# Optimization experiments

Measured on AMD Instinct MI355X. Metric: run time of the kernel, lower is better.

The kernel has to match this reference:

```python
import jax, jax.numpy as jnp
import numpy as np

NUM_HEADS = 16
HIDDEN = 1024
HEAD_DIM = HIDDEN // NUM_HEADS


def setup_inputs() -> dict:
    key = jax.random.key(0)
    ks = jax.random.split(key, 12)
    B, S, H = 4, 1024, HIDDEN
    s = 1.0 / np.sqrt(H)
    inp = {
        "aspect_hidden": jax.random.normal(ks[0], (B, S, H), jnp.float32),
        "opinion_hidden": jax.random.normal(ks[1], (B, S, H), jnp.float32),
        "attention_mask": jnp.ones((B, S), jnp.int32),
        # torch nn.Linear weights are [out, in]
        "Wq": jax.random.normal(ks[2], (H, H), jnp.float32) * s,
        "bq": jnp.zeros((H,), jnp.float32),
        "Wk": jax.random.normal(ks[3], (H, H), jnp.float32) * s,
        "bk": jnp.zeros((H,), jnp.float32),
        "Wv": jax.random.normal(ks[4], (H, H), jnp.float32) * s,
        "bv": jnp.zeros((H,), jnp.float32),
        "Wo": jax.random.normal(ks[5], (H, H), jnp.float32) * s,
        "bo": jnp.zeros((H,), jnp.float32),
        # nn.Bilinear(H, H, 1): weight [1, H, H], bias [1]
        "Wbil": jax.random.normal(ks[6], (1, H, H), jnp.float32) * s,
        "bbil": jnp.zeros((1,), jnp.float32),
    }
    return inp


def reference(aspect_hidden, opinion_hidden, attention_mask,
              Wq, bq, Wk, bk, Wv, bv, Wo, bo, Wbil, bbil):
    B, Sq, H = aspect_hidden.shape
    Sk = opinion_hidden.shape[1]
    nh, hd = NUM_HEADS, HEAD_DIM
    scale = hd ** (-0.5)

    q = (aspect_hidden @ Wq.T + bq).reshape(B, Sq, nh, hd).transpose(0, 2, 1, 3)
    k = (opinion_hidden @ Wk.T + bk).reshape(B, Sk, nh, hd).transpose(0, 2, 1, 3)
    v = (opinion_hidden @ Wv.T + bv).reshape(B, Sk, nh, hd).transpose(0, 2, 1, 3)

    # bilinear span bias: span[b,s] = a[b,s] @ Wbil[0] @ o[b,s] + bbil
    span = jnp.einsum('bsh,hk,bsk->bs', aspect_hidden, Wbil[0], opinion_hidden) + bbil[0]

    # scores [B, nh, Sq, Sk] with span bias broadcast over heads and keys
    scores = jnp.einsum('bhqd,bhkd->bhqk', q, k) * scale + span[:, None, :, None]
    scores = jnp.where(attention_mask[:, None, None, :] == 0, -jnp.inf, scores)

    probs = jax.nn.softmax(scores, axis=-1)
    ctx = jnp.einsum('bhqk,bhkd->bhqd', probs, v)
    ctx = ctx.transpose(0, 2, 1, 3).reshape(B, Sq, H)
    return ctx @ Wo.T + bo
```

## Files before the change

kernel.cpp:

```cpp
#include <hip/hip_runtime.h>
#include <hip/hip_bf16.h>
#include <stdint.h>

typedef __attribute__((ext_vector_type(4))) float f32x4;
typedef __attribute__((ext_vector_type(16))) float f32x16;
typedef __attribute__((ext_vector_type(8))) short bf16x8;
typedef __attribute__((ext_vector_type(4))) unsigned int u32x4;
typedef unsigned short u16;

#define GBL_AS1(p) ((const __attribute__((address_space(1))) void*)(p))
#define LDS_AS3(p) ((__attribute__((address_space(3))) void*)(p))

static __device__ __forceinline__ u16 f2bf(float f) {
  __hip_bfloat16 h = __float2bfloat16(f);
  union { __hip_bfloat16 h; u16 u; } c; c.h = h;
  return c.u;
}

__global__ __launch_bounds__(256) void fused_cast(
    const float* __restrict__ a, const float* __restrict__ o,
    const float* __restrict__ wq_, const float* __restrict__ wk_,
    const float* __restrict__ wv_, const float* __restrict__ wo_,
    const int* __restrict__ mask,
    u16* __restrict__ aB, u16* __restrict__ oB,
    u16* __restrict__ WqB, u16* __restrict__ WkB,
    u16* __restrict__ WvB, u16* __restrict__ WoB,
    int* __restrict__ flags) {
  if (blockIdx.x == 0 && threadIdx.x < 64) {
    int bb = threadIdx.x >> 4, kt = threadIdx.x & 15;
    int anyz = 0;
    for (int s = 0; s < 64; ++s) anyz |= (mask[bb * 1024 + kt * 64 + s] == 0);
    flags[threadIdx.x] = anyz;
  }
  int idx = blockIdx.x * 256 + threadIdx.x;
#pragma unroll
  for (int j = 0; j < 4; ++j) {
    int i = idx + j * 786432;
    const float* src; u16* dst; int off;
    if (i < 1048576) { src = a; dst = aB; off = i; }
    else if (i < 2097152) { src = o; dst = oB; off = i - 1048576; }
    else {
      int w = (i - 2097152) >> 18; off = (i - 2097152) & 262143;
      src = (w == 0) ? wq_ : (w == 1) ? wk_ : (w == 2) ? wv_ : wo_;
      dst = (w == 0) ? WqB : (w == 1) ? WkB : (w == 2) ? WvB : WoB;
    }
    float4 v = reinterpret_cast<const float4*>(src)[off];
    ushort4 ov;
    ov.x = f2bf(v.x); ov.y = f2bf(v.y); ov.z = f2bf(v.z); ov.w = f2bf(v.w);
    reinterpret_cast<ushort4*>(dst)[off] = ov;
  }
}

static __device__ __forceinline__ void gemm_core2(const u16* __restrict__ A,
                                                  const u16* __restrict__ B,
                                                  u16* lds_a, u16* lds_b,
                                                  f32x4 acc[4][4]) {
  const int tid = threadIdx.x, lane = tid & 63, wv = tid >> 6;
  const int wm = wv >> 1, wn = wv & 1;
  const int fr = lane & 15, fq = lane >> 4;

#define GSTAGE(kt_, buf_) do { \
    _Pragma("unroll") \
    for (int i_ = 0; i_ < 4; ++i_) { \
      int cb_ = (wv * 4 + i_) * 64; \
      int c_ = cb_ + lane; \
      int r_ = c_ >> 3; \
      int sc_ = ((c_ & 7) ^ (r_ & 7)) * 8; \
      __builtin_amdgcn_global_load_lds(GBL_AS1(A + (size_t)r_ * 1024 + (kt_) * 64 + sc_), \
                                       LDS_AS3(lds_a + (buf_) * 8192 + cb_ * 8), 16, 0, 0); \
      __builtin_amdgcn_global_load_lds(GBL_AS1(B + (size_t)r_ * 1024 + (kt_) * 64 + sc_), \
                                       LDS_AS3(lds_b + (buf_) * 8192 + cb_ * 8), 16, 0, 0); \
    } \
  } while (0)

  GSTAGE(0, 0);
  __syncthreads();
  for (int kt = 0; kt < 16; ++kt) {
    const int cur = kt & 1;
    if (kt < 15) GSTAGE(kt + 1, cur ^ 1);
    const u16* la = lds_a + cur * 8192;
    const u16* lb = lds_b + cur * 8192;
#pragma unroll
    for (int ks = 0; ks < 2; ++ks) {
      bf16x8 af[4], bfv[4];
#pragma unroll
      for (int mi = 0; mi < 4; ++mi) {
        int r = wm * 64 + mi * 16 + fr;
        af[mi] = *(const bf16x8*)&la[r * 64 + (((ks * 4 + fq) ^ (r & 7)) * 8)];
      }
#pragma unroll
      for (int ni = 0; ni < 4; ++ni) {
        int r = wn * 64 + ni * 16 + fr;
        bfv[ni] = *(const bf16x8*)&lb[r * 64 + (((ks * 4 + fq) ^ (r & 7)) * 8)];
      }
#pragma unroll
      for (int mi = 0; mi < 4; ++mi)
#pragma unroll
        for (int ni = 0; ni < 4; ++ni)
          acc[mi][ni] = __builtin_amdgcn_mfma_f32_16x16x32_bf16(af[mi], bfv[ni], acc[mi][ni], 0, 0, 0);
    }
    __syncthreads();
  }
#undef GSTAGE
}

__global__ __launch_bounds__(256, 2) void qkv_gemm(
    const u16* __restrict__ aB, const u16* __restrict__ oB,
    const u16* __restrict__ Wq, const u16* __restrict__ Wk, const u16* __restrict__ Wv,
    const float* __restrict__ bq, const float* __restrict__ bk, const float* __restrict__ bv,
    u16* __restrict__ q_ws, u16* __restrict__ k_ws, u16* __restrict__ vt_ws) {
  __shared__ __align__(16) u16 lds_a[2 * 128 * 64];
  __shared__ __align__(16) u16 lds_b[2 * 128 * 64];
  const int mt = blockIdx.x;
  const int nt = blockIdx.y;
  const int w = nt >> 3, ntl = nt & 7;
  const u16* A = (w == 0) ? aB : oB;
  const u16* W = (w == 0) ? Wq : (w == 1) ? Wk : Wv;
  const float* bias = (w == 0) ? bq : (w == 1) ? bk : bv;
  f32x4 acc[4][4];
#pragma unroll
  for (int i = 0; i < 4; ++i)
#pragma unroll
    for (int j = 0; j < 4; ++j) acc[i][j] = (f32x4){0.f, 0.f, 0.f, 0.f};
  gemm_core2(A + (size_t)mt * 128 * 1024, W + (size_t)ntl * 128 * 1024, lds_a, lds_b, acc);
  const int lane = threadIdx.x & 63, wvi = threadIdx.x >> 6;
  const int wm = wvi >> 1, wn = wvi & 1, fr = lane & 15, fq = lane >> 4;
  u16* dst01 = (w == 0) ? q_ws : k_ws;
  const float qscl = (w == 0) ? 0.18033688f : 1.0f;
#pragma unroll
  for (int mi = 0; mi < 4; ++mi)
#pragma unroll
    for (int ni = 0; ni < 4; ++ni)
#pragma unroll
      for (int r = 0; r < 4; ++r) {
        int m = mt * 128 + wm * 64 + mi * 16 + fq * 4 + r;
        int nl = ntl * 128 + wn * 64 + ni * 16 + fr;
        float v = (acc[mi][ni][r] + bias[nl]) * qscl;
        int b = m >> 10, s = m & 1023, h = nl >> 6, d = nl & 63;
        u16 u = f2bf(v);
        if (w < 2) dst01[(((size_t)(b * 16 + h)) * 1024 + s) * 64 + d] = u;
        else       vt_ws[(((size_t)(b * 16 + h)) * 64 + d) * 1024 + s] = u;
      }
}

__global__ __launch_bounds__(256, 4) void attn_kernel(
    const u16* __restrict__ q_ws, const u16* __restrict__ k_ws,
    const u16* __restrict__ vt_ws, const int* __restrict__ mask,
    const int* __restrict__ flags, u16* __restrict__ ctx_ws) {
  __shared__ __align__(16) u16 k_lds[2][64 * 64];
  __shared__ __align__(16) u16 vt_lds[2][64 * 64];
  __shared__ __align__(16) float scl_lds[4][32];
  const int bid = blockIdx.x;
  const int bh = bid & 63, qt = bid >> 6;
  const int b = bh >> 4, h = bh & 15;
  const int tid = threadIdx.x, lane = tid & 63, wv = tid >> 6;
  const int l31 = lane & 31, hi = lane >> 5;
  const u16* qbase = q_ws + (size_t)bh * 65536 + (size_t)qt * 8192;
  const u16* kbase = k_ws + (size_t)bh * 65536;
  const u16* vtbase = vt_ws + (size_t)bh * 65536;

#define STAGE_KV(kt_, buf_) do { \
    _Pragma("unroll") \
    for (int i_ = 0; i_ < 2; ++i_) { \
      int cb_ = (wv * 2 + i_) * 64; \
      int c_ = cb_ + lane; \
      int r_ = c_ >> 3; \
      int sc_ = ((c_ & 7) ^ (r_ & 7)) * 8; \
      __builtin_amdgcn_global_load_lds(GBL_AS1(kbase + (size_t)((kt_) * 64 + r_) * 64 + sc_), \
                                       LDS_AS3(&k_lds[buf_][cb_ * 8]), 16, 0, 0); \
      __builtin_amdgcn_global_load_lds(GBL_AS1(vtbase + (size_t)r_ * 1024 + (kt_) * 64 + sc_), \
                                       LDS_AS3(&vt_lds[buf_][cb_ * 8]), 16, 0, 0); \
    } \
  } while (0)

  {
    u16* qstage = &k_lds[0][0];
#pragma unroll
    for (int i_ = 0; i_ < 4; ++i_) {
      int cb_ = (wv * 4 + i_) * 64;
      int c_ = cb_ + lane;
      int r_ = c_ >> 3;
      int sc_ = ((c_ & 7) ^ (r_ & 7)) * 8;
      __builtin_amdgcn_global_load_lds(GBL_AS1(qbase + (size_t)r_ * 64 + sc_),
                                       LDS_AS3(qstage + cb_ * 8), 16, 0, 0);
    }
  }
  __syncthreads();
  bf16x8 qf[4];
  {
    int rq = wv * 32 + l31;
    const u16* qr = &k_lds[0][0] + rq * 64;
    int rx = rq & 7;
#pragma unroll
    for (int ds = 0; ds < 4; ++ds)
      qf[ds] = *(const bf16x8*)&qr[((ds * 2 + hi) ^ rx) * 8];
  }
  __syncthreads();
  STAGE_KV(0, 0);
  __syncthreads();

  f32x16 ctx0, ctx1;
#pragma unroll
  for (int z = 0; z < 16; ++z) { ctx0[z] = 0.f; ctx1[z] = 0.f; }
  float mrow = -1e30f, lrow = 0.f;

  for (int kt = 0; kt < 16; ++kt) {
    const int cur = kt & 1;
    if (kt < 15) STAGE_KV(kt + 1, cur ^ 1);

    f32x16 sc[2];
#pragma unroll
    for (int kb = 0; kb < 2; ++kb) {
      f32x16 a;
#pragma unroll
      for (int z = 0; z < 16; ++z) a[z] = 0.f;
      int r = kb * 32 + l31;
      const u16* kr = &k_lds[cur][r * 64];
      int rx = r & 7;
#pragma unroll
      for (int ds = 0; ds < 4; ++ds) {
        bf16x8 kf = *(const bf16x8*)&kr[((ds * 2 + hi) ^ rx) * 8];
        a = __builtin_amdgcn_mfma_f32_32x32x16_bf16(kf, qf[ds], a, 0, 0, 0);
      }
      sc[kb] = a;
    }

    if (flags[b * 16 + kt]) {
#pragma unroll
      for (int kb = 0; kb < 2; ++kb)
#pragma unroll
        for (int r2 = 0; r2 < 16; ++r2) {
          int key = kb * 32 + (r2 & 3) + 8 * (r2 >> 2) + 4 * hi;
          if (mask[b * 1024 + kt * 64 + key] == 0) sc[kb][r2] = -30000.0f;
        }
    }

    float pmax = -3.0e38f;
#pragma unroll
    for (int kb = 0; kb < 2; ++kb)
#pragma unroll
      for (int r2 = 0; r2 < 16; ++r2) pmax = fmaxf(pmax, sc[kb][r2]);
    pmax = fmaxf(pmax, __shfl_xor(pmax, 32));

    if (__any(pmax > mrow + 8.0f)) {
      float mnew = fmaxf(mrow, pmax);
      float scl = __builtin_exp2f(mrow - mnew);
      mrow = mnew;
      lrow *= scl;
      if (hi == 0) scl_lds[wv][l31] = scl;
      asm volatile("s_waitcnt lgkmcnt(0)" ::: "memory");
#pragma unroll
      for (int g = 0; g < 4; ++g) {
        float4 s4 = *(const float4*)&scl_lds[wv][g * 8 + hi * 4];
        const float* sp = (const float*)&s4;
#pragma unroll
        for (int i2 = 0; i2 < 4; ++i2) {
          ctx0[g * 4 + i2] *= sp[i2];
          ctx1[g * 4 + i2] *= sp[i2];
        }
      }
    }

    float psum = 0.f;
#pragma unroll
    for (int kb = 0; kb < 2; ++kb)
#pragma unroll
      for (int r2 = 0; r2 < 16; ++r2) {
        float p = __builtin_exp2f(sc[kb][r2] - mrow);
        sc[kb][r2] = p;
        psum += p;
      }
    psum += __shfl_xor(psum, 32);
    lrow += psum;

#pragma unroll
    for (int kb = 0; kb < 2; ++kb) {
      unsigned int w[8];
#pragma unroll
      for (int j = 0; j < 8; ++j) {
        unsigned int t;
        asm("v_cvt_pk_bf16_f32 %0, %1, %2" : "=v"(t) : "v"(sc[kb][2 * j]), "v"(sc[kb][2 * j + 1]));
        w[j] = t;
      }
      unsigned int sw0 = (unsigned)__shfl_xor((int)w[0], 32), sw1 = (unsigned)__shfl_xor((int)w[1], 32);
      unsigned int sw2 = (unsigned)__shfl_xor((int)w[2], 32), sw3 = (unsigned)__shfl_xor((int)w[3], 32);
      unsigned int sw4 = (unsigned)__shfl_xor((int)w[4], 32), sw5 = (unsigned)__shfl_xor((int)w[5], 32);
      unsigned int sw6 = (unsigned)__shfl_xor((int)w[6], 32), sw7 = (unsigned)__shfl_xor((int)w[7], 32);
      union { u32x4 u; bf16x8 b; } P0, P1;
      P0.u = (u32x4){ hi ? sw2 : w[0], hi ? sw3 : w[1], hi ? w[2] : sw0, hi ? w[3] : sw1 };
      P1.u = (u32x4){ hi ? sw6 : w[4], hi ? sw7 : w[5], hi ? w[6] : sw4, hi ? w[7] : sw5 };
#pragma unroll
      for (int db = 0; db < 2; ++db) {
        int rv = db * 32 + l31;
        const u16* vr = &vt_lds[cur][rv * 64];
        int rvx = rv & 7;
        bf16x8 v0 = *(const bf16x8*)&vr[((kb * 4 + hi) ^ rvx) * 8];
        bf16x8 v1 = *(const bf16x8*)&vr[((kb * 4 + 2 + hi) ^ rvx) * 8];
        if (db == 0) {
          ctx0 = __builtin_amdgcn_mfma_f32_32x32x16_bf16(P0.b, v0, ctx0, 0, 0, 0);
          ctx0 = __builtin_amdgcn_mfma_f32_32x32x16_bf16(P1.b, v1, ctx0, 0, 0, 0);
        } else {
          ctx1 = __builtin_amdgcn_mfma_f32_32x32x16_bf16(P0.b, v0, ctx1, 0, 0, 0);
          ctx1 = __builtin_amdgcn_mfma_f32_32x32x16_bf16(P1.b, v1, ctx1, 0, 0, 0);
        }
      }
    }
    __syncthreads();
  }

  float inv = (lrow > 0.f) ? 1.0f / lrow : 0.f;
  if (hi == 0) scl_lds[wv][l31] = inv;
  asm volatile("s_waitcnt lgkmcnt(0)" ::: "memory");
  const int sbase = qt * 128 + wv * 32;
#pragma unroll
  for (int g = 0; g < 4; ++g) {
    float4 s4 = *(const float4*)&scl_lds[wv][g * 8 + hi * 4];
    const float* sp = (const float*)&s4;
#pragma unroll
    for (int i2 = 0; i2 < 4; ++i2) {
      int s = sbase + g * 8 + hi * 4 + i2;
      size_t rowoff = ((size_t)(b * 1024 + s)) * 1024 + h * 64;
      ctx_ws[rowoff + l31]      = f2bf(ctx0[g * 4 + i2] * sp[i2]);
      ctx_ws[rowoff + 32 + l31] = f2bf(ctx1[g * 4 + i2] * sp[i2]);
    }
  }
#undef STAGE_KV
}

__global__ __launch_bounds__(256, 2) void out_gemm(const u16* __restrict__ ctxB,
                                                   const u16* __restrict__ Wo,
                                                   const float* __restrict__ bo,
                                                   float* __restrict__ out) {
  __shared__ __align__(16) u16 lds_a[2 * 128 * 64];
  __shared__ __align__(16) u16 lds_b[2 * 128 * 64];
  const int mt = blockIdx.x, nt = blockIdx.y;
  f32x4 acc[4][4];
#pragma unroll
  for (int i = 0; i < 4; ++i)
#pragma unroll
    for (int j = 0; j < 4; ++j) acc[i][j] = (f32x4){0.f, 0.f, 0.f, 0.f};
  gemm_core2(ctxB + (size_t)mt * 128 * 1024, Wo + (size_t)nt * 128 * 1024, lds_a, lds_b, acc);
  const int lane = threadIdx.x & 63, wvi = threadIdx.x >> 6;
  const int wm = wvi >> 1, wn = wvi & 1, fr = lane & 15, fq = lane >> 4;
#pragma unroll
  for (int mi = 0; mi < 4; ++mi)
#pragma unroll
    for (int ni = 0; ni < 4; ++ni)
#pragma unroll
      for (int r = 0; r < 4; ++r) {
        int m = mt * 128 + wm * 64 + mi * 16 + fq * 4 + r;
        int n = nt * 128 + wn * 64 + ni * 16 + fr;
        out[(size_t)m * 1024 + n] = acc[mi][ni][r] + bo[n];
      }
}

extern "C" void kernel_launch(void* const* d_in, const int* in_sizes, int n_in,
                              void* d_out, int out_size, void* d_ws, size_t ws_size,
                              hipStream_t stream) {
  const float* aspect = (const float*)d_in[0];
  const float* opinion = (const float*)d_in[1];
  const int* mask = (const int*)d_in[2];
  const float* Wq = (const float*)d_in[3];
  const float* bq = (const float*)d_in[4];
  const float* Wk = (const float*)d_in[5];
  const float* bk = (const float*)d_in[6];
  const float* Wv = (const float*)d_in[7];
  const float* bv = (const float*)d_in[8];
  const float* Wo = (const float*)d_in[9];
  const float* bo = (const float*)d_in[10];
  float* out = (float*)d_out;
  char* ws = (char*)d_ws;

  const size_t MB = 1u << 20;
  u16* aB    = (u16*)(ws + 0 * MB);
  u16* oB    = (u16*)(ws + 8 * MB);
  u16* WqB   = (u16*)(ws + 16 * MB);
  u16* WkB   = (u16*)(ws + 18 * MB);
  u16* WvB   = (u16*)(ws + 20 * MB);
  u16* WoB   = (u16*)(ws + 22 * MB);
  u16* q_ws  = (u16*)(ws + 24 * MB);
  u16* k_ws  = (u16*)(ws + 32 * MB);
  u16* vt_ws = (u16*)(ws + 40 * MB);
  u16* ctx_ws= (u16*)(ws + 48 * MB);
  int* flags = (int*)(out + out_size - 64);

  fused_cast<<<3072, 256, 0, stream>>>(aspect, opinion, Wq, Wk, Wv, Wo, mask,
                                       aB, oB, WqB, WkB, WvB, WoB, flags);
  qkv_gemm<<<dim3(32, 24), 256, 0, stream>>>(aB, oB, WqB, WkB, WvB, bq, bk, bv,
                                             q_ws, k_ws, vt_ws);
  attn_kernel<<<512, 256, 0, stream>>>(q_ws, k_ws, vt_ws, mask, flags, ctx_ws);
  out_gemm<<<dim3(32, 8), 256, 0, stream>>>(ctx_ws, WoB, bo, out);
}
```

Before: 120.3 us.

## Replace QKV GEMM with 256x256-tile 8-wave kernel using phased LDS pipeline

The QKV projection GEMM moves from 128x128 tiles with 4 waves to 256x256 tiles with 8 waves. Each wave computes a 128x64 sub-tile in quadrant phases, and global-to-LDS loads are split into quarter-tile stages interleaved with the MFMA phases, using explicit waitcnt, barriers and setprio. This raises arithmetic intensity per LDS byte and overlaps loads with compute. The trade-off is a grid of only 192 blocks, which may leave some CUs underused on a 256-CU part, plus 128KB of LDS per block and high register pressure.

Result: slower. 135.8 us (+12.9%).

```diff
diff --git a/kernel.cpp b/kernel.cpp
--- a/kernel.cpp
+++ b/kernel.cpp
@@ -51,6 +51,139 @@
   }
 }
 
+__global__ __launch_bounds__(512, 2) void qkv_gemm8(
+    const u16* __restrict__ aB, const u16* __restrict__ oB,
+    const u16* __restrict__ Wq, const u16* __restrict__ Wk, const u16* __restrict__ Wv,
+    const float* __restrict__ bq, const float* __restrict__ bk, const float* __restrict__ bv,
+    u16* __restrict__ q_ws, u16* __restrict__ k_ws, u16* __restrict__ vt_ws) {
+  __shared__ __align__(16) u16 lA[2][256 * 64];
+  __shared__ __align__(16) u16 lB[2][256 * 64];
+  const int mt = blockIdx.x, nt = blockIdx.y;
+  const int w = nt >> 2;
+  const u16* Asrc = (w == 0) ? aB : oB;
+  const u16* Bsrc = ((w == 0) ? Wq : (w == 1) ? Wk : Wv) + (size_t)(nt & 3) * 256 * 1024;
+  const u16* Abase = Asrc + (size_t)mt * 256 * 1024;
+  const float* bias = (w == 0) ? bq : (w == 1) ? bk : bv;
+
+  const int tid = threadIdx.x, lane = tid & 63, wid = tid >> 6;
+  const int wr = wid >> 2, wc = wid & 3;
+  const int fr = lane & 15, fq = lane >> 4;
+
+  int srcoff[2], dstoff[2];
+#pragma unroll
+  for (int i = 0; i < 2; ++i) {
+    int p = (wid * 2 + i) * 64 + lane;
+    int rp = p >> 3, cp = p & 7;
+    int lc = cp ^ (rp & 7);
+    srcoff[i] = rp * 1024 + lc * 8;
+    dstoff[i] = (wid * 2 + i) * 512;
+  }
+
+#define STAGE_H(kt_, h_) do { \
+    const u16* s_ = ((h_) < 2) ? Abase : Bsrc; \
+    u16* d_ = (((h_) < 2) ? &lA[(kt_) & 1][0] : &lB[(kt_) & 1][0]) + ((h_) & 1) * 8192; \
+    _Pragma("unroll") \
+    for (int i_ = 0; i_ < 2; ++i_) \
+      __builtin_amdgcn_global_load_lds( \
+          GBL_AS1(s_ + (size_t)((h_) & 1) * 131072 + (size_t)(kt_) * 64 + srcoff[i_]), \
+          LDS_AS3(d_ + dstoff[i_]), 16, 0, 0); \
+  } while (0)
+
+#define READ_A(qm_) do { \
+    _Pragma("unroll") \
+    for (int m4 = 0; m4 < 4; ++m4) { \
+      int row = wr * 128 + ((qm_) * 4 + m4) * 16 + fr; \
+      _Pragma("unroll") \
+      for (int ks = 0; ks < 2; ++ks) \
+        af[m4][ks] = *(const bf16x8*)&lA[cur][row * 64 + (((ks * 4 + fq) ^ (fr & 7)) * 8)]; \
+    } \
+  } while (0)
+
+#define READ_B(qn_) do { \
+    _Pragma("unroll") \
+    for (int n2 = 0; n2 < 2; ++n2) { \
+      int row = wc * 64 + ((qn_) * 2 + n2) * 16 + fr; \
+      _Pragma("unroll") \
+      for (int ks = 0; ks < 2; ++ks) \
+        bfr[n2][ks] = *(const bf16x8*)&lB[cur][row * 64 + (((ks * 4 + fq) ^ (fr & 7)) * 8)]; \
+    } \
+  } while (0)
+
+  f32x4 acc[8][4];
+#pragma unroll
+  for (int i = 0; i < 8; ++i)
+#pragma unroll
+    for (int j = 0; j < 4; ++j) acc[i][j] = (f32x4){0.f, 0.f, 0.f, 0.f};
+
+  bf16x8 af[4][2], bfr[2][2];
+
+  STAGE_H(0, 0); STAGE_H(0, 1); STAGE_H(0, 2); STAGE_H(0, 3);
+
+  for (int it = 0; it < 8; ++it) {
+#pragma unroll
+    for (int ph = 0; ph < 8; ++ph) {
+      const int cur = ph >> 2;
+      const int sub = ph & 3;
+      const int qm = (ph >> 1) & 1;
+      const int qn = (ph & 1) ^ qm;
+      const int st = it * 2 + 1 + (ph >> 2);
+
+      if (sub == 0) {
+        if (st < 16) {
+          STAGE_H(st, 0);
+          asm volatile("s_waitcnt vmcnt(2)" ::: "memory");
+        } else {
+          asm volatile("s_waitcnt vmcnt(0)" ::: "memory");
+        }
+        __builtin_amdgcn_s_barrier();
+        __builtin_amdgcn_sched_barrier(0);
+        READ_A(qm); READ_B(qn);
+      } else {
+        if (sub == 1) READ_B(qn);
+        else if (sub == 2) READ_A(qm);
+        else READ_B(qn);
+        if (st < 16) STAGE_H(st, sub);
+        __builtin_amdgcn_s_barrier();
+      }
+      asm volatile("s_waitcnt lgkmcnt(0)" ::: "memory");
+      __builtin_amdgcn_sched_barrier(0);
+      __builtin_amdgcn_s_setprio(1);
+#pragma unroll
+      for (int m4 = 0; m4 < 4; ++m4)
+#pragma unroll
+        for (int n2 = 0; n2 < 2; ++n2)
+#pragma unroll
+          for (int ks = 0; ks < 2; ++ks)
+            acc[qm * 4 + m4][qn * 2 + n2] = __builtin_amdgcn_mfma_f32_16x16x32_bf16(
+                af[m4][ks], bfr[n2][ks], acc[qm * 4 + m4][qn * 2 + n2], 0, 0, 0);
+      __builtin_amdgcn_s_setprio(0);
+      __builtin_amdgcn_s_barrier();
+    }
+  }
+
+  u16* dst01 = (w == 0) ? q_ws : k_ws;
+  const float qscl = (w == 0) ? 0.18033688f : 1.0f;
+#pragma unroll
+  for (int mi = 0; mi < 8; ++mi)
+#pragma unroll
+    for (int ni = 0; ni < 4; ++ni) {
+      int n = (nt & 3) * 256 + wc * 64 + ni * 16 + fr;
+      int h = n >> 6, d = n & 63;
+      float bv_ = bias[n];
+#pragma unroll
+      for (int r = 0; r < 4; ++r) {
+        int m = mt * 256 + wr * 128 + mi * 16 + fq * 4 + r;
+        int b = m >> 10, s = m & 1023;
+        u16 u = f2bf((acc[mi][ni][r] + bv_) * qscl);
+        if (w < 2) dst01[(((size_t)(b * 16 + h)) * 1024 + s) * 64 + d] = u;
+        else       vt_ws[(((size_t)(b * 16 + h)) * 64 + d) * 1024 + s] = u;
+      }
+    }
+#undef STAGE_H
+#undef READ_A
+#undef READ_B
+}
+
 static __device__ __forceinline__ void gemm_core2(const u16* __restrict__ A,
                                                   const u16* __restrict__ B,
                                                   u16* lds_a, u16* lds_b,
@@ -102,45 +235,6 @@
     __syncthreads();
   }
 #undef GSTAGE
-}
-
-__global__ __launch_bounds__(256, 2) void qkv_gemm(
-    const u16* __restrict__ aB, const u16* __restrict__ oB,
-    const u16* __restrict__ Wq, const u16* __restrict__ Wk, const u16* __restrict__ Wv,
-    const float* __restrict__ bq, const float* __restrict__ bk, const float* __restrict__ bv,
-    u16* __restrict__ q_ws, u16* __restrict__ k_ws, u16* __restrict__ vt_ws) {
-  __shared__ __align__(16) u16 lds_a[2 * 128 * 64];
-  __shared__ __align__(16) u16 lds_b[2 * 128 * 64];
-  const int mt = blockIdx.x;
-  const int nt = blockIdx.y;
-  const int w = nt >> 3, ntl = nt & 7;
-  const u16* A = (w == 0) ? aB : oB;
-  const u16* W = (w == 0) ? Wq : (w == 1) ? Wk : Wv;
-  const float* bias = (w == 0) ? bq : (w == 1) ? bk : bv;
-  f32x4 acc[4][4];
-#pragma unroll
-  for (int i = 0; i < 4; ++i)
-#pragma unroll
-    for (int j = 0; j < 4; ++j) acc[i][j] = (f32x4){0.f, 0.f, 0.f, 0.f};
-  gemm_core2(A + (size_t)mt * 128 * 1024, W + (size_t)ntl * 128 * 1024, lds_a, lds_b, acc);
-  const int lane = threadIdx.x & 63, wvi = threadIdx.x >> 6;
-  const int wm = wvi >> 1, wn = wvi & 1, fr = lane & 15, fq = lane >> 4;
-  u16* dst01 = (w == 0) ? q_ws : k_ws;
-  const float qscl = (w == 0) ? 0.18033688f : 1.0f;
-#pragma unroll
-  for (int mi = 0; mi < 4; ++mi)
-#pragma unroll
-    for (int ni = 0; ni < 4; ++ni)
-#pragma unroll
-      for (int r = 0; r < 4; ++r) {
-        int m = mt * 128 + wm * 64 + mi * 16 + fq * 4 + r;
-        int nl = ntl * 128 + wn * 64 + ni * 16 + fr;
-        float v = (acc[mi][ni][r] + bias[nl]) * qscl;
-        int b = m >> 10, s = m & 1023, h = nl >> 6, d = nl & 63;
-        u16 u = f2bf(v);
-        if (w < 2) dst01[(((size_t)(b * 16 + h)) * 1024 + s) * 64 + d] = u;
-        else       vt_ws[(((size_t)(b * 16 + h)) * 64 + d) * 1024 + s] = u;
-      }
 }
 
 __global__ __launch_bounds__(256, 4) void attn_kernel(
@@ -386,8 +480,8 @@
 
   fused_cast<<<3072, 256, 0, stream>>>(aspect, opinion, Wq, Wk, Wv, Wo, mask,
                                        aB, oB, WqB, WkB, WvB, WoB, flags);
-  qkv_gemm<<<dim3(32, 24), 256, 0, stream>>>(aB, oB, WqB, WkB, WvB, bq, bk, bv,
-                                             q_ws, k_ws, vt_ws);
+  qkv_gemm8<<<dim3(16, 12), 512, 0, stream>>>(aB, oB, WqB, WkB, WvB, bq, bk, bv,
+                                              q_ws, k_ws, vt_ws);
   attn_kernel<<<512, 256, 0, stream>>>(q_ws, k_ws, vt_ws, mask, flags, ctx_ws);
   out_gemm<<<dim3(32, 8), 256, 0, stream>>>(ctx_ws, WoB, bo, out);
 }
```
